# Kernel tuning notes

Hardware: AMD Instinct MI355X
Metric: run time of the kernel (lower is better)

Reference implementation:

```python
import jax, jax.numpy as jnp
import numpy as np

DIM = 1024
HEADS = 16
HEAD_DIM = DIM // HEADS
SCALE = HEAD_DIM ** -0.5
EPS_R = 1e-8
EPS_LN = 1e-5


def setup_inputs() -> dict:
    key = jax.random.key(0)
    ks = jax.random.split(key, 8)
    B, L = 4, 2048
    tokens = jax.random.normal(ks[0], (B, L, DIM), dtype=jnp.float32)
    R = jax.random.uniform(ks[1], (L, L), dtype=jnp.float32)
    s = DIM ** -0.5
    Wq = jax.random.normal(ks[2], (DIM, DIM), dtype=jnp.float32) * s
    Wk = jax.random.normal(ks[3], (DIM, DIM), dtype=jnp.float32) * s
    Wv = jax.random.normal(ks[4], (DIM, DIM), dtype=jnp.float32) * s
    Wp = jax.random.normal(ks[5], (DIM, DIM), dtype=jnp.float32) * s
    beta = jnp.ones((1,), dtype=jnp.float32)
    gamma = jnp.ones((DIM,), dtype=jnp.float32)
    bias = jnp.zeros((DIM,), dtype=jnp.float32)
    return {"tokens": tokens, "R": R, "Wq": Wq, "Wk": Wk, "Wv": Wv,
            "Wp": Wp, "beta": beta, "gamma": gamma, "bias": bias}


def reference(tokens, R, Wq, Wk, Wv, Wp, beta, gamma, bias):
    B, L, D = tokens.shape
    H, Dh = HEADS, HEAD_DIM
    residual = tokens
    # nn.Linear(bias=False): y = x @ W.T
    Q = (tokens @ Wq.T).reshape(B, L, H, Dh).transpose(0, 2, 1, 3)  # [B,H,L,Dh]
    K = (tokens @ Wk.T).reshape(B, L, H, Dh).transpose(0, 2, 1, 3)
    V = (tokens @ Wv.T).reshape(B, L, H, Dh).transpose(0, 2, 1, 3)
    attn = jnp.einsum('bhqd,bhkd->bhqk', Q, K) * SCALE
    log_R = jnp.log(jnp.maximum(R, EPS_R))  # [L,L]
    attn = attn + beta[0] * log_R[None, None, :, :]
    attn = jax.nn.softmax(attn, axis=-1)
    out = jnp.einsum('bhqk,bhkd->bhqd', attn, V)
    out = out.transpose(0, 2, 1, 3).reshape(B, L, D)
    out = out @ Wp.T
    x = out + residual
    mu = jnp.mean(x, axis=-1, keepdims=True)
    var = jnp.mean(jnp.square(x - mu), axis=-1, keepdims=True)
    return (x - mu) * jax.lax.rsqrt(var + EPS_LN) * gamma + bias
```

## Files before the change

kernel.cpp:

```cpp
#include <hip/hip_runtime.h>

#define DEV __device__ __forceinline__

typedef __attribute__((ext_vector_type(4))) float f32x4;
typedef __attribute__((ext_vector_type(16))) float f32x16;
typedef __attribute__((ext_vector_type(8))) short bf8v;
typedef __attribute__((ext_vector_type(4))) unsigned short u16x4;
typedef __attribute__((ext_vector_type(8))) unsigned short u16x8;
typedef __attribute__((ext_vector_type(2))) unsigned int u32x2;

static constexpr int LSEQ = 2048;
static constexpr int DIM  = 1024;
static constexpr int NH   = 16;
static constexpr int DH   = 64;
static constexpr int NB   = 4;
static constexpr int MROWS = NB * LSEQ;
static constexpr float QSCALE = 0.18033688011112042f;

DEV unsigned short f2bf(float x) {
  unsigned u = __float_as_uint(x);
  return (unsigned short)((u + 0x7fffu + ((u >> 16) & 1u)) >> 16);
}

DEV unsigned cvt_pk_bf16(float a, float b) {
  unsigned r;
  asm("v_cvt_pk_bf16_f32 %0, %1, %2" : "=v"(r) : "v"(a), "v"(b));
  return r;
}

DEV void pl32swap(unsigned& a, unsigned& b) {
  asm("v_permlane32_swap_b32 %0, %1" : "+v"(a), "+v"(b));
}

DEV float fexp2(float x) {
  float r;
  asm("v_exp_f32 %0, %1" : "=v"(r) : "v"(x));
  return r;
}

DEV void gload_lds16(const void* g, void* l) {
  __builtin_amdgcn_global_load_lds((const __attribute__((address_space(1))) void*)g,
                                   (__attribute__((address_space(3))) void*)l, 16, 0, 0);
}

__global__ __launch_bounds__(256) void k_cvt(const float* __restrict__ src,
                                             unsigned short* __restrict__ dst, int n) {
  int i = (blockIdx.x * 256 + threadIdx.x) * 8;
  if (i >= n) return;
  f32x4 a = *(const f32x4*)(src + i);
  f32x4 b = *(const f32x4*)(src + i + 4);
  u16x8 o;
  o[0] = f2bf(a[0]); o[1] = f2bf(a[1]); o[2] = f2bf(a[2]); o[3] = f2bf(a[3]);
  o[4] = f2bf(b[0]); o[5] = f2bf(b[1]); o[6] = f2bf(b[2]); o[7] = f2bf(b[3]);
  *(u16x8*)(dst + i) = o;
}

__global__ __launch_bounds__(256) void k_rbx(const float* __restrict__ R,
                                             const float* __restrict__ beta,
                                             u16x4* __restrict__ out) {
  __shared__ u16x4 lds2[2048];
  const int tid = threadIdx.x;
  const int q0 = blockIdx.x * 128;
  const int t  = blockIdx.y;
  const float b = beta[0];
  #pragma unroll
  for (int it = 0; it < 4; ++it) {
    int ql = it * 32 + (tid >> 3);
    int kl = (tid & 7) * 8;
    const float* src = R + (size_t)(q0 + ql) * 2048 + t * 64 + kl;
    f32x4 v0 = *(const f32x4*)src;
    f32x4 v1 = *(const f32x4*)(src + 4);
    u16x4 qa, qb;
    #pragma unroll
    for (int m = 0; m < 4; ++m) {
      qa[m] = f2bf(exp2f(b * log2f(fmaxf(v0[m], 1e-8f))));
      qb[m] = f2bf(exp2f(b * log2f(fmaxf(v1[m], 1e-8f))));
    }
    int s = kl >> 4, w = (kl >> 3) & 1;
    lds2[(((s * 2 + 0) * 128) + ql) * 2 + w] = qa;
    lds2[(((s * 2 + 1) * 128) + ql) * 2 + w] = qb;
  }
  __syncthreads();
  u16x8* O = (u16x8*)out;
  #pragma unroll
  for (int j = 0; j < 4; ++j) {
    int f = j * 256 + tid;
    int r = f >> 7, qrel = f & 127;
    O[(size_t)(t * 8 + r) * 2048 + q0 + qrel] = *(const u16x8*)&lds2[(r * 128 + qrel) * 2];
  }
}

DEV void gemm_core(const unsigned short* __restrict__ A, const unsigned short* __restrict__ Bm,
                   int m0, int n0, unsigned short* As, unsigned short* Bs, f32x4 (*acc)[4]) {
  const int tid = threadIdx.x;
  const int lane = tid & 63, wid = tid >> 6;
  const int g = lane >> 4, lq = lane & 15;
  const int wr = wid >> 1, wc = wid & 1;

  int aoff[2][4], boff[2][4];
  #pragma unroll
  for (int kk = 0; kk < 2; ++kk) {
    #pragma unroll
    for (int t = 0; t < 4; ++t) {
      aoff[kk][t] = (((wr * 64 + t * 16 + lq) * 128 + kk * 64 + g * 16) ^ ((lq & 7) << 4));
      boff[kk][t] = (((wc * 64 + t * 16 + lq) * 128 + kk * 64 + g * 16) ^ ((lq & 7) << 4));
    }
  }

  for (int kt = 0; kt < 16; ++kt) {
    #pragma unroll
    for (int i = 0; i < 4; ++i) {
      int chunk = i * 256 + tid;
      int row = chunk >> 3;
      int cc = (chunk & 7) ^ (row & 7);
      gload_lds16(A + (size_t)(m0 + row) * 1024 + kt * 64 + cc * 8, As + (i * 256 + wid * 64) * 8);
      gload_lds16(Bm + (size_t)(n0 + row) * 1024 + kt * 64 + cc * 8, Bs + (i * 256 + wid * 64) * 8);
    }
    __syncthreads();
    #pragma unroll
    for (int kk = 0; kk < 2; ++kk) {
      bf8v af[4], bfr[4];
      #pragma unroll
      for (int mi = 0; mi < 4; ++mi) af[mi] = *(const bf8v*)((const char*)As + aoff[kk][mi]);
      #pragma unroll
      for (int ni = 0; ni < 4; ++ni) bfr[ni] = *(const bf8v*)((const char*)Bs + boff[kk][ni]);
      #pragma unroll
      for (int mi = 0; mi < 4; ++mi)
        #pragma unroll
        for (int ni = 0; ni < 4; ++ni)
          acc[mi][ni] = __builtin_amdgcn_mfma_f32_16x16x32_bf16(af[mi], bfr[ni], acc[mi][ni], 0, 0, 0);
    }
    __syncthreads();
  }
}

__global__ __launch_bounds__(256) void k_gemm_qkv(
    const unsigned short* __restrict__ A, const unsigned short* __restrict__ W,
    unsigned short* __restrict__ Qb, unsigned short* __restrict__ Kb,
    unsigned short* __restrict__ Vt) {
  __shared__ unsigned short As[128 * 64];
  __shared__ unsigned short Bs[128 * 64];
  f32x4 acc[4][4];
  f32x4 z = {0.f, 0.f, 0.f, 0.f};
  #pragma unroll
  for (int mi = 0; mi < 4; ++mi)
    #pragma unroll
    for (int ni = 0; ni < 4; ++ni) acc[mi][ni] = z;

  const int m0 = blockIdx.x * 128, n0 = blockIdx.y * 128;
  gemm_core(A, W, m0, n0, As, Bs, acc);

  const int tid = threadIdx.x;
  const int lane = tid & 63, wid = tid >> 6;
  const int g = lane >> 4, lq = lane & 15;
  const int wr = wid >> 1, wc = wid & 1;
  const int region = n0 >> 10;
  const int nrel0 = n0 & 1023;

  if (region < 2) {
    unsigned short* dst = (region == 0) ? Qb : Kb;
    const float sc = (region == 0) ? QSCALE : 1.0f;
    #pragma unroll
    for (int mi = 0; mi < 4; ++mi)
      #pragma unroll
      for (int ni = 0; ni < 4; ++ni) {
        int m = m0 + wr * 64 + mi * 16 + g * 4;
        int n = nrel0 + wc * 64 + ni * 16 + lq;
        int b = m >> 11, l = m & 2047;
        int h = n >> 6, d = n & 63;
        int base = ((b * NH + h) * LSEQ + l) * DH + d;
        #pragma unroll
        for (int r = 0; r < 4; ++r)
          dst[base + r * DH] = f2bf(acc[mi][ni][r] * sc);
      }
  } else {
    #pragma unroll
    for (int mi = 0; mi < 4; ++mi)
      #pragma unroll
      for (int ni = 0; ni < 4; ++ni) {
        int m = m0 + wr * 64 + mi * 16 + g * 4;
        int n = nrel0 + wc * 64 + ni * 16 + lq;
        int b = m >> 11, l = m & 2047;
        int h = n >> 6, d = n & 63;
        u16x4 pk;
        #pragma unroll
        for (int r = 0; r < 4; ++r) pk[r] = f2bf(acc[mi][ni][r]);
        *(u16x4*)(Vt + (size_t)((b * NH + h) * DH + d) * LSEQ + l) = pk;
      }
  }
}

__global__ __launch_bounds__(256, 4) void k_attn(
    const unsigned short* __restrict__ Qb, const unsigned short* __restrict__ Kb,
    const unsigned short* __restrict__ Vt, const unsigned short* __restrict__ RbX,
    unsigned short* __restrict__ AO) {
  __shared__ unsigned short Ks[2][64 * 64];
  __shared__ unsigned short Vs[2][64 * 64];
  const int tid = threadIdx.x;
  const int lane = tid & 63, wid = tid >> 6;
  const int l32 = lane & 31, hi = lane >> 5;
  const int bh = blockIdx.y;
  const int q0 = blockIdx.x * 128;
  const int b = bh >> 4, h = bh & 15;
  const char* Kbh = (const char*)(Kb + (size_t)bh * LSEQ * DH);
  const char* Vbh = (const char*)(Vt + (size_t)bh * DH * LSEQ);
  const int qw = q0 + wid * 32;
  const int q = qw + l32;

  const unsigned short* Qbh = Qb + (size_t)bh * LSEQ * DH;
  bf8v qf[4];
  #pragma unroll
  for (int s = 0; s < 4; ++s)
    qf[s] = *(const bf8v*)(Qbh + (size_t)q * DH + s * 16 + hi * 8);

  f32x16 oacc[2];
  #pragma unroll
  for (int db = 0; db < 2; ++db)
    #pragma unroll
    for (int r = 0; r < 16; ++r) oacc[db][r] = 0.f;
  float mrun = -__builtin_inff();
  float lrun = 0.f;

  const unsigned rb_off = (unsigned)(hi * 2048 + q) * 16u;
  int koffs[2], voffs[2], ldso[2];
  #pragma unroll
  for (int i = 0; i < 2; ++i) {
    int chunk = i * 256 + tid;
    int row = chunk >> 3;
    int cc = (chunk & 7) ^ (row & 7);
    koffs[i] = row * (DH * 2) + cc * 16;
    voffs[i] = row * (LSEQ * 2) + cc * 16;
    ldso[i]  = (i * 256 + wid * 64) * 16;
  }

  #pragma unroll
  for (int i = 0; i < 2; ++i) {
    gload_lds16(Kbh + koffs[i], (char*)Ks[0] + ldso[i]);
    gload_lds16(Vbh + voffs[i], (char*)Vs[0] + ldso[i]);
  }
  __syncthreads();

  auto TILE = [&](int t, int buf, bool pref) {
    const char* rb_t = (const char*)RbX + (size_t)t * 262144;
    u16x8 rr01[2];
    rr01[0] = *(const u16x8*)(rb_t + rb_off);
    rr01[1] = *(const u16x8*)(rb_t + 65536 + rb_off);

    if (pref) {
      const char* Kt = Kbh + (size_t)(t + 1) * (64 * DH * 2);
      const char* Vt_ = Vbh + (size_t)(t + 1) * (64 * 2);
      #pragma unroll
      for (int i = 0; i < 2; ++i) {
        gload_lds16(Kt + koffs[i], (char*)Ks[buf ^ 1] + ldso[i]);
        gload_lds16(Vt_ + voffs[i], (char*)Vs[buf ^ 1] + ldso[i]);
      }
    }

    f32x16 sac[2];
    #pragma unroll
    for (int r = 0; r < 16; ++r) { sac[0][r] = 0.f; sac[1][r] = 0.f; }
    __builtin_amdgcn_s_setprio(1);
    #pragma unroll
    for (int s = 0; s < 4; ++s) {
      #pragma unroll
      for (int kb2 = 0; kb2 < 2; ++kb2) {
        int row = kb2 * 32 + l32;
        bf8v kf = *(const bf8v*)((const char*)Ks[buf] +
                   ((row * 128 + s * 32 + hi * 16) ^ ((row & 7) << 4)));
        sac[kb2] = __builtin_amdgcn_mfma_f32_32x32x16_bf16(kf, qf[s], sac[kb2], 0, 0, 0);
      }
    }
    __builtin_amdgcn_s_setprio(0);

    u16x8 rr23[2];
    rr23[0] = *(const u16x8*)(rb_t + 131072 + rb_off);
    rr23[1] = *(const u16x8*)(rb_t + 196608 + rb_off);

    float mx;
    {
      float m8[8];
      #pragma unroll
      for (int j = 0; j < 8; ++j)
        m8[j] = fmaxf(fmaxf(sac[0][2 * j], sac[0][2 * j + 1]),
                      fmaxf(sac[1][2 * j], sac[1][2 * j + 1]));
      float m4a = fmaxf(m8[0], m8[1]), m4b = fmaxf(m8[2], m8[3]);
      float m4c = fmaxf(m8[4], m8[5]), m4d = fmaxf(m8[6], m8[7]);
      mx = fmaxf(fmaxf(m4a, m4b), fmaxf(m4c, m4d));
      mx = fmaxf(mx, __shfl_xor(mx, 32));
    }

    if (__any(mx > mrun + 8.f)) {
      float mnew = fmaxf(mrun, mx);
      float corr = fexp2(mrun - mnew);
      mrun = mnew;
      lrun *= corr;
      #pragma unroll
      for (int db = 0; db < 2; ++db)
        #pragma unroll
        for (int r = 0; r < 16; ++r) oacc[db][r] *= corr;
    }

    float ls = 0.f;
    auto SLICE = [&](int s, u16x8 rv) {
      const int blk = s >> 1, r0 = 8 * (s & 1);
      float p[8];
      #pragma unroll
      for (int i = 0; i < 8; ++i) {
        float rf = __uint_as_float((unsigned)(unsigned short)rv[i] << 16);
        p[i] = fexp2(sac[blk][r0 + i] - mrun) * rf;
      }
      ls += ((p[0] + p[1]) + (p[2] + p[3])) + ((p[4] + p[5]) + (p[6] + p[7]));
      unsigned w0 = cvt_pk_bf16(p[0], p[1]);
      unsigned w2 = cvt_pk_bf16(p[4], p[5]);
      unsigned w1 = cvt_pk_bf16(p[2], p[3]);
      unsigned w3 = cvt_pk_bf16(p[6], p[7]);
      pl32swap(w0, w2);
      pl32swap(w1, w3);
      union { unsigned w[4]; bf8v v; } pf;
      pf.w[0] = w0; pf.w[1] = w1; pf.w[2] = w2; pf.w[3] = w3;
      #pragma unroll
      for (int db = 0; db < 2; ++db) {
        int row = db * 32 + l32;
        bf8v vf = *(const bf8v*)((const char*)Vs[buf] +
                   ((row * 128 + s * 32 + hi * 16) ^ ((row & 7) << 4)));
        oacc[db] = __builtin_amdgcn_mfma_f32_32x32x16_bf16(vf, pf.v, oacc[db], 0, 0, 0);
      }
    };
    SLICE(0, rr01[0]); SLICE(1, rr01[1]); SLICE(2, rr23[0]); SLICE(3, rr23[1]);
    ls += __shfl_xor(ls, 32);
    lrun += ls;
    __syncthreads();
  };

  for (int tp = 0; tp < 16; ++tp) {
    TILE(2 * tp,     0, true);
    TILE(2 * tp + 1, 1, tp != 15);
  }

  float inv = 1.f / lrun;
  #pragma unroll
  for (int db = 0; db < 2; ++db)
    #pragma unroll
    for (int u = 0; u < 4; ++u) {
      u32x2 w;
      w[0] = cvt_pk_bf16(oacc[db][4 * u + 0] * inv, oacc[db][4 * u + 1] * inv);
      w[1] = cvt_pk_bf16(oacc[db][4 * u + 2] * inv, oacc[db][4 * u + 3] * inv);
      int d = db * 32 + u * 8 + hi * 4;
      *(u32x2*)(AO + (size_t)(b * LSEQ + q) * DIM + h * DH + d) = w;
    }
}

__global__ __launch_bounds__(256) void k_gemm_proj(
    const unsigned short* __restrict__ A, const unsigned short* __restrict__ W,
    const float* __restrict__ res, float* __restrict__ out) {
  __shared__ unsigned short As[128 * 64];
  __shared__ unsigned short Bs[128 * 64];
  f32x4 acc[4][4];
  f32x4 z = {0.f, 0.f, 0.f, 0.f};
  #pragma unroll
  for (int mi = 0; mi < 4; ++mi)
    #pragma unroll
    for (int ni = 0; ni < 4; ++ni) acc[mi][ni] = z;

  const int m0 = blockIdx.x * 128, n0 = blockIdx.y * 128;
  gemm_core(A, W, m0, n0, As, Bs, acc);

  const int tid = threadIdx.x;
  const int lane = tid & 63, wid = tid >> 6;
  const int g = lane >> 4, lq = lane & 15;
  const int wr = wid >> 1, wc = wid & 1;
  #pragma unroll
  for (int mi = 0; mi < 4; ++mi)
    #pragma unroll
    for (int ni = 0; ni < 4; ++ni) {
      int m = m0 + wr * 64 + mi * 16 + g * 4;
      int n = n0 + wc * 64 + ni * 16 + lq;
      #pragma unroll
      for (int r = 0; r < 4; ++r) {
        int idx = (m + r) * 1024 + n;
        out[idx] = acc[mi][ni][r] + res[idx];
      }
    }
}

__global__ __launch_bounds__(256) void k_ln(float* __restrict__ x,
                                            const float* __restrict__ gamma,
                                            const float* __restrict__ bias) {
  const int row = blockIdx.x;
  const int tid = threadIdx.x;
  float* xr = x + (size_t)row * 1024;
  f32x4 v = *(f32x4*)(xr + tid * 4);
  float s = v[0] + v[1] + v[2] + v[3];
  float ss = v[0] * v[0] + v[1] * v[1] + v[2] * v[2] + v[3] * v[3];
  #pragma unroll
  for (int off = 1; off < 64; off <<= 1) {
    s += __shfl_xor(s, off);
    ss += __shfl_xor(ss, off);
  }
  __shared__ float red[8];
  const int lane = tid & 63, wid = tid >> 6;
  if (lane == 0) { red[wid] = s; red[wid + 4] = ss; }
  __syncthreads();
  s = red[0] + red[1] + red[2] + red[3];
  ss = red[4] + red[5] + red[6] + red[7];
  float mu = s * (1.f / 1024.f);
  float var = ss * (1.f / 1024.f) - mu * mu;
  float rs = rsqrtf(var + 1e-5f);
  f32x4 gm = *(const f32x4*)(gamma + tid * 4);
  f32x4 bi = *(const f32x4*)(bias + tid * 4);
  f32x4 o;
  #pragma unroll
  for (int j = 0; j < 4; ++j) o[j] = (v[j] - mu) * rs * gm[j] + bi[j];
  *(f32x4*)(xr + tid * 4) = o;
}

extern "C" void kernel_launch(void* const* d_in, const int* in_sizes, int n_in,
                              void* d_out, int out_size, void* d_ws, size_t ws_size,
                              hipStream_t stream) {
  const float* tokens = (const float*)d_in[0];
  const float* R      = (const float*)d_in[1];
  const float* Wq     = (const float*)d_in[2];
  const float* Wk     = (const float*)d_in[3];
  const float* Wv     = (const float*)d_in[4];
  const float* Wp     = (const float*)d_in[5];
  const float* beta   = (const float*)d_in[6];
  const float* gamma  = (const float*)d_in[7];
  const float* bias   = (const float*)d_in[8];
  float* out = (float*)d_out;
  char* ws = (char*)d_ws;

  unsigned short* tok_bf = (unsigned short*)(ws);
  unsigned short* wqkv   = (unsigned short*)(ws + 16777216);
  unsigned short* wp     = (unsigned short*)(ws + 23068672);
  u16x4*          rbx    = (u16x4*)(ws + 25165824);
  unsigned short* qb     = (unsigned short*)(ws + 41943040);
  unsigned short* kb     = (unsigned short*)(ws + 58720256);
  unsigned short* vt     = (unsigned short*)(ws + 75497472);
  unsigned short* ao     = tok_bf;

  k_cvt<<<4096, 256, 0, stream>>>(tokens, tok_bf, MROWS * DIM);
  k_cvt<<<512, 256, 0, stream>>>(Wq, wqkv, DIM * DIM);
  k_cvt<<<512, 256, 0, stream>>>(Wk, wqkv + DIM * DIM, DIM * DIM);
  k_cvt<<<512, 256, 0, stream>>>(Wv, wqkv + 2 * DIM * DIM, DIM * DIM);
  k_cvt<<<512, 256, 0, stream>>>(Wp, wp, DIM * DIM);
  k_rbx<<<dim3(16, 32), 256, 0, stream>>>(R, beta, rbx);

  k_gemm_qkv<<<dim3(64, 24), 256, 0, stream>>>(tok_bf, wqkv, qb, kb, vt);
  k_attn<<<dim3(16, 64), 256, 0, stream>>>(qb, kb, vt, (const unsigned short*)rbx, ao);
  k_gemm_proj<<<dim3(64, 8), 256, 0, stream>>>(ao, wp, tokens, out);
  k_ln<<<8192, 256, 0, stream>>>(out, gamma, bias);
}
```

Measured before the change: 246.6 us.

## Merge weight conversions into one launch and pack attention softmax math

```diff
diff --git a/kernel.cpp b/kernel.cpp
--- a/kernel.cpp
+++ b/kernel.cpp
@@ -2,12 +2,14 @@
 
 #define DEV __device__ __forceinline__
 
+typedef __attribute__((ext_vector_type(2))) float f32x2;
 typedef __attribute__((ext_vector_type(4))) float f32x4;
 typedef __attribute__((ext_vector_type(16))) float f32x16;
 typedef __attribute__((ext_vector_type(8))) short bf8v;
 typedef __attribute__((ext_vector_type(4))) unsigned short u16x4;
 typedef __attribute__((ext_vector_type(8))) unsigned short u16x8;
 typedef __attribute__((ext_vector_type(2))) unsigned int u32x2;
+typedef __attribute__((ext_vector_type(4))) unsigned int u32x4;
 
 static constexpr int LSEQ = 2048;
 static constexpr int DIM  = 1024;
@@ -55,6 +57,22 @@
   *(u16x8*)(dst + i) = o;
 }
 
+__global__ __launch_bounds__(256) void k_cvtw(const float* __restrict__ w0,
+                                              const float* __restrict__ w1,
+                                              const float* __restrict__ w2,
+                                              const float* __restrict__ w3,
+                                              unsigned short* __restrict__ dst) {
+  int r = blockIdx.x >> 9;
+  const float* src = (r == 0) ? w0 : (r == 1) ? w1 : (r == 2) ? w2 : w3;
+  int i = ((blockIdx.x & 511) * 256 + threadIdx.x) * 8;
+  f32x4 a = *(const f32x4*)(src + i);
+  f32x4 b = *(const f32x4*)(src + i + 4);
+  u16x8 o;
+  o[0] = f2bf(a[0]); o[1] = f2bf(a[1]); o[2] = f2bf(a[2]); o[3] = f2bf(a[3]);
+  o[4] = f2bf(b[0]); o[5] = f2bf(b[1]); o[6] = f2bf(b[2]); o[7] = f2bf(b[3]);
+  *(u16x8*)(dst + (size_t)r * DIM * DIM + i) = o;
+}
+
 __global__ __launch_bounds__(256) void k_rbx(const float* __restrict__ R,
                                              const float* __restrict__ beta,
                                              u16x4* __restrict__ out) {
@@ -222,38 +240,33 @@
   float lrun = 0.f;
 
   const unsigned rb_off = (unsigned)(hi * 2048 + q) * 16u;
-  int koffs[2], voffs[2], ldso[2];
-  #pragma unroll
-  for (int i = 0; i < 2; ++i) {
-    int chunk = i * 256 + tid;
-    int row = chunk >> 3;
-    int cc = (chunk & 7) ^ (row & 7);
-    koffs[i] = row * (DH * 2) + cc * 16;
-    voffs[i] = row * (LSEQ * 2) + cc * 16;
-    ldso[i]  = (i * 256 + wid * 64) * 16;
-  }
-
-  #pragma unroll
-  for (int i = 0; i < 2; ++i) {
-    gload_lds16(Kbh + koffs[i], (char*)Ks[0] + ldso[i]);
-    gload_lds16(Vbh + voffs[i], (char*)Vs[0] + ldso[i]);
-  }
+  int koff, voff, ldso;
+  {
+    int row = tid >> 3;
+    int cc = (tid & 7) ^ (row & 7);
+    koff = row * (DH * 2) + cc * 16;
+    voff = row * (LSEQ * 2) + cc * 16;
+    ldso = (wid * 64) * 16;
+  }
+
+  gload_lds16(Kbh + koff, (char*)Ks[0] + ldso);
+  gload_lds16(Kbh + koff + 4096, (char*)Ks[0] + ldso + 4096);
+  gload_lds16(Vbh + voff, (char*)Vs[0] + ldso);
+  gload_lds16(Vbh + voff + 131072, (char*)Vs[0] + ldso + 4096);
   __syncthreads();
 
   auto TILE = [&](int t, int buf, bool pref) {
     const char* rb_t = (const char*)RbX + (size_t)t * 262144;
-    u16x8 rr01[2];
-    rr01[0] = *(const u16x8*)(rb_t + rb_off);
-    rr01[1] = *(const u16x8*)(rb_t + 65536 + rb_off);
+    u32x4 rrA = *(const u32x4*)(rb_t + rb_off);
+    u32x4 rrB = *(const u32x4*)(rb_t + 65536 + rb_off);
 
     if (pref) {
       const char* Kt = Kbh + (size_t)(t + 1) * (64 * DH * 2);
-      const char* Vt_ = Vbh + (size_t)(t + 1) * (64 * 2);
-      #pragma unroll
-      for (int i = 0; i < 2; ++i) {
-        gload_lds16(Kt + koffs[i], (char*)Ks[buf ^ 1] + ldso[i]);
-        gload_lds16(Vt_ + voffs[i], (char*)Vs[buf ^ 1] + ldso[i]);
-      }
+      const char* Vn = Vbh + (size_t)(t + 1) * (64 * 2);
+      gload_lds16(Kt + koff, (char*)Ks[buf ^ 1] + ldso);
+      gload_lds16(Kt + koff + 4096, (char*)Ks[buf ^ 1] + ldso + 4096);
+      gload_lds16(Vn + voff, (char*)Vs[buf ^ 1] + ldso);
+      gload_lds16(Vn + voff + 131072, (char*)Vs[buf ^ 1] + ldso + 4096);
     }
 
     f32x16 sac[2];
@@ -271,10 +284,6 @@
       }
     }
     __builtin_amdgcn_s_setprio(0);
-
-    u16x8 rr23[2];
-    rr23[0] = *(const u16x8*)(rb_t + 131072 + rb_off);
-    rr23[1] = *(const u16x8*)(rb_t + 196608 + rb_off);
 
     float mx;
     {
@@ -300,24 +309,28 @@
         for (int r = 0; r < 16; ++r) oacc[db][r] *= corr;
     }
 
-    float ls = 0.f;
-    auto SLICE = [&](int s, u16x8 rv) {
+    f32x2 m2; m2[0] = mrun; m2[1] = mrun;
+    f32x2 ls2; ls2[0] = 0.f; ls2[1] = 0.f;
+
+    auto SLICE = [&](int s, const u32x4& rv) {
       const int blk = s >> 1, r0 = 8 * (s & 1);
-      float p[8];
-      #pragma unroll
-      for (int i = 0; i < 8; ++i) {
-        float rf = __uint_as_float((unsigned)(unsigned short)rv[i] << 16);
-        p[i] = fexp2(sac[blk][r0 + i] - mrun) * rf;
-      }
-      ls += ((p[0] + p[1]) + (p[2] + p[3])) + ((p[4] + p[5]) + (p[6] + p[7]));
-      unsigned w0 = cvt_pk_bf16(p[0], p[1]);
-      unsigned w2 = cvt_pk_bf16(p[4], p[5]);
-      unsigned w1 = cvt_pk_bf16(p[2], p[3]);
-      unsigned w3 = cvt_pk_bf16(p[6], p[7]);
-      pl32swap(w0, w2);
-      pl32swap(w1, w3);
-      union { unsigned w[4]; bf8v v; } pf;
-      pf.w[0] = w0; pf.w[1] = w1; pf.w[2] = w2; pf.w[3] = w3;
+      unsigned w[4];
+      #pragma unroll
+      for (int i = 0; i < 4; ++i) {
+        f32x2 sv; sv[0] = sac[blk][r0 + 2 * i]; sv[1] = sac[blk][r0 + 2 * i + 1];
+        sv = sv - m2;
+        f32x2 pe; pe[0] = fexp2(sv[0]); pe[1] = fexp2(sv[1]);
+        f32x2 rf;
+        rf[0] = __uint_as_float(rv[i] << 16);
+        rf[1] = __uint_as_float(rv[i] & 0xffff0000u);
+        pe = pe * rf;
+        ls2 = ls2 + pe;
+        w[i] = cvt_pk_bf16(pe[0], pe[1]);
+      }
+      pl32swap(w[0], w[2]);
+      pl32swap(w[1], w[3]);
+      union { unsigned u[4]; bf8v v; } pf;
+      pf.u[0] = w[0]; pf.u[1] = w[1]; pf.u[2] = w[2]; pf.u[3] = w[3];
       #pragma unroll
       for (int db = 0; db < 2; ++db) {
         int row = db * 32 + l32;
@@ -326,7 +339,13 @@
         oacc[db] = __builtin_amdgcn_mfma_f32_32x32x16_bf16(vf, pf.v, oacc[db], 0, 0, 0);
       }
     };
-    SLICE(0, rr01[0]); SLICE(1, rr01[1]); SLICE(2, rr23[0]); SLICE(3, rr23[1]);
+    SLICE(0, rrA);
+    rrA = *(const u32x4*)(rb_t + 131072 + rb_off);
+    SLICE(1, rrB);
+    rrB = *(const u32x4*)(rb_t + 196608 + rb_off);
+    SLICE(2, rrA);
+    SLICE(3, rrB);
+    float ls = ls2[0] + ls2[1];
     ls += __shfl_xor(ls, 32);
     lrun += ls;
     __syncthreads();
@@ -439,10 +458,7 @@
   unsigned short* ao     = tok_bf;
 
   k_cvt<<<4096, 256, 0, stream>>>(tokens, tok_bf, MROWS * DIM);
-  k_cvt<<<512, 256, 0, stream>>>(Wq, wqkv, DIM * DIM);
-  k_cvt<<<512, 256, 0, stream>>>(Wk, wqkv + DIM * DIM, DIM * DIM);
-  k_cvt<<<512, 256, 0, stream>>>(Wv, wqkv + 2 * DIM * DIM, DIM * DIM);
-  k_cvt<<<512, 256, 0, stream>>>(Wp, wp, DIM * DIM);
+  k_cvtw<<<2048, 256, 0, stream>>>(Wq, Wk, Wv, Wp, wqkv);
   k_rbx<<<dim3(16, 32), 256, 0, stream>>>(R, beta, rbx);
 
   k_gemm_qkv<<<dim3(64, 24), 256, 0, stream>>>(tok_bf, wqkv, qb, kb, vt);
```

New measurement: 235.4 us. -4.5%, faster.
